# Kernel optimization log

Hardware: AMD Instinct MI355X
Metric: run time of the kernel (lower is better)

## Reference

```python
import jax, jax.numpy as jnp
import numpy as np

EPS = 1e-5  # torch InstanceNorm2d default eps


def instance_norm(x):
    # normalize over spatial dims (H, W) per sample, per channel; affine=False
    mean = jnp.mean(x, axis=(2, 3), keepdims=True)
    var = jnp.var(x, axis=(2, 3), keepdims=True)  # biased var, matching torch
    return (x - mean) * jax.lax.rsqrt(var + EPS)


def conv1x1(x, w, b):
    # x: [B,C,H,W], w: [O,C], b: [O] -> [B,O,H,W]
    return jnp.einsum('oc,bchw->bohw', w, x) + b[None, :, None, None]


def setup_inputs() -> dict:
    key = jax.random.key(0)
    ks = jax.random.split(key, 9)
    B, C, H, W = 4, 64, 96, 96
    fan_out = C  # 1x1 conv: fan_out = out_ch * 1 * 1
    std = float(np.sqrt(2.0 / fan_out))  # kaiming_normal_, mode='fan_out', relu
    x = jax.random.normal(ks[0], (B, C, H, W), dtype=jnp.float32)
    wq = jax.random.normal(ks[1], (C, C), dtype=jnp.float32) * std
    wk = jax.random.normal(ks[2], (C, C), dtype=jnp.float32) * std
    wv = jax.random.normal(ks[3], (C, C), dtype=jnp.float32) * std
    wo = jax.random.normal(ks[4], (C, C), dtype=jnp.float32) * std
    bq = jnp.zeros((C,), dtype=jnp.float32)
    bk = jnp.zeros((C,), dtype=jnp.float32)
    bv = jnp.zeros((C,), dtype=jnp.float32)
    bo = jnp.zeros((C,), dtype=jnp.float32)
    return {"x": x, "wq": wq, "bq": bq, "wk": wk, "bk": bk,
            "wv": wv, "bv": bv, "wo": wo, "bo": bo}


def reference(x, wq, bq, wk, bk, wv, bv, wo, bo):
    B, C, H, W = x.shape
    h = instance_norm(x)
    q = conv1x1(h, wq, bq)  # [B,C,H,W]
    k = conv1x1(h, wk, bk)
    v = conv1x1(h, wv, bv)
    N = H * W
    q = q.reshape(B, C, N).transpose(0, 2, 1)  # [B,N,C]
    k = k.reshape(B, C, N)                     # [B,C,N]
    v = v.reshape(B, C, N).transpose(0, 2, 1)  # [B,N,C]
    scores = jnp.einsum('bnc,bcm->bnm', q, k) * (C ** -0.5)  # [B,N,N]
    attn = jax.nn.softmax(scores, axis=-1)
    o = jnp.einsum('bnm,bmc->bnc', attn, v)  # [B,N,C]
    o = o.reshape(B, H, W, C).transpose(0, 3, 1, 2)  # [B,C,H,W]
    o = conv1x1(o, wo, bo)
    return x + o
```

## Files before the change

### kernel.cpp

```cpp
#include <hip/hip_runtime.h>
#include <stdint.h>

#define BB 4
#define CCH 64
#define NN 9216
#define NTILES 144
#define FTILES 72
#define NCHUNK 3
#define CHUNKK 3072

typedef unsigned short u16;
typedef __attribute__((ext_vector_type(8))) short bhalf8;
typedef __attribute__((ext_vector_type(4))) float f32x4;
typedef __attribute__((ext_vector_type(4))) u16 u16x4;
typedef __attribute__((ext_vector_type(8))) u16 u16x8;
typedef __attribute__((ext_vector_type(2))) unsigned int u32x2;

#define MFMA16(a, b, c) __builtin_amdgcn_mfma_f32_16x16x32_bf16((a), (b), (c), 0, 0, 0)

static __device__ __forceinline__ u16 f2bf(float f) {
  union { float f; unsigned u; } v; v.f = f;
  return (u16)((v.u + 0x7fffu + ((v.u >> 16) & 1u)) >> 16);
}
static __device__ __forceinline__ float bf2f(u16 h) {
  union { unsigned u; float f; } v; v.u = ((unsigned)h) << 16; return v.f;
}
static __device__ __forceinline__ unsigned pk2(float lo, float hi) {
  unsigned a = __float_as_uint(hi) + 0x8000u;
  unsigned b = __float_as_uint(lo) + 0x8000u;
  return __builtin_amdgcn_perm(a, b, 0x07060302u);
}
static __device__ __forceinline__ void glds16(const void* g, void* l) {
  __builtin_amdgcn_global_load_lds(
      (const __attribute__((address_space(1))) unsigned int*)g,
      (__attribute__((address_space(3))) unsigned int*)l, 16, 0, 0);
}

extern "C" __global__ __launch_bounds__(256) void prep_kernel(
    const float* __restrict__ x,
    const float* __restrict__ wq, const float* __restrict__ wk,
    const float* __restrict__ wv, const float* __restrict__ wo,
    float* __restrict__ mean, float* __restrict__ rstd, u16* __restrict__ wbf) {
  if (blockIdx.x >= 256) {
    int i = (blockIdx.x - 256) * 256 + threadIdx.x;
    const float* src = (i < 4096) ? wq : (i < 8192) ? wk : (i < 12288) ? wv : wo;
    wbf[i] = f2bf(src[i & 4095]);
    return;
  }
  int idx = blockIdx.x;
  const float* p = x + (size_t)idx * NN;
  float s = 0.f, ss = 0.f;
  for (int i = threadIdx.x; i < NN; i += 256) { float v = p[i]; s += v; ss += v * v; }
#pragma unroll
  for (int o = 32; o > 0; o >>= 1) { s += __shfl_xor(s, o, 64); ss += __shfl_xor(ss, o, 64); }
  __shared__ float ls[4], lss[4];
  int w = threadIdx.x >> 6;
  if ((threadIdx.x & 63) == 0) { ls[w] = s; lss[w] = ss; }
  __syncthreads();
  if (threadIdx.x == 0) {
    s = ls[0] + ls[1] + ls[2] + ls[3];
    ss = lss[0] + lss[1] + lss[2] + lss[3];
    float m = s * (1.f / NN);
    float var = ss * (1.f / NN) - m * m;
    mean[idx] = m;
    rstd[idx] = rsqrtf(var + 1e-5f);
  }
}

extern "C" __global__ __launch_bounds__(256, 4) void qkv_kernel(
    const float* __restrict__ x,
    const float* __restrict__ mean, const float* __restrict__ rstd,
    const u16* __restrict__ wqb, const u16* __restrict__ wkb, const u16* __restrict__ wvb,
    const float* __restrict__ bq, const float* __restrict__ bk,
    u16* __restrict__ Qt, u16* __restrict__ Kt, u16* __restrict__ Vt) {
  __shared__ u16 hbuf[64 * 72];
  int b = blockIdx.x / NTILES, tile = blockIdx.x % NTILES;
  int n0 = tile * 64;
  int t = threadIdx.x;
  int w = t >> 6, lane = t & 63, q = lane >> 4, ln = lane & 15;
  const float QSCALE = 0.125f * 1.44269504088896340736f;
  const float* mb = mean + b * 64;
  const float* rb_ = rstd + b * 64;
  int nloc = lane;
#pragma unroll
  for (int rep = 0; rep < 4; rep++) {
    int c0 = 16 * w + 4 * rep;
    float h0 = (x[(size_t)(b * 64 + c0 + 0) * NN + n0 + nloc] - mb[c0 + 0]) * rb_[c0 + 0];
    float h1 = (x[(size_t)(b * 64 + c0 + 1) * NN + n0 + nloc] - mb[c0 + 1]) * rb_[c0 + 1];
    float h2 = (x[(size_t)(b * 64 + c0 + 2) * NN + n0 + nloc] - mb[c0 + 2]) * rb_[c0 + 2];
    float h3 = (x[(size_t)(b * 64 + c0 + 3) * NN + n0 + nloc] - mb[c0 + 3]) * rb_[c0 + 3];
    u32x2 hp;
    hp[0] = pk2(h0, h1);
    hp[1] = pk2(h2, h3);
    *(u32x2*)&hbuf[nloc * 72 + c0] = hp;
  }
  __syncthreads();
  int hrow = (16 * w + ln) * 72;
  bhalf8 hb0 = *(const bhalf8*)&hbuf[hrow + q * 8];
  bhalf8 hb1 = *(const bhalf8*)&hbuf[hrow + 32 + q * 8];
  size_t nrow = (size_t)(b * NN + n0 + 16 * w + ln) * 64;
#pragma unroll
  for (int ct = 0; ct < 4; ct++) {
    int wrow = (16 * ct + ln) * 64;
    bhalf8 a0 = *(const bhalf8*)&wqb[wrow + q * 8];
    bhalf8 a1 = *(const bhalf8*)&wqb[wrow + 32 + q * 8];
    f32x4 d = {0.f, 0.f, 0.f, 0.f};
    d = MFMA16(a0, hb0, d);
    d = MFMA16(a1, hb1, d);
    f32x4 b4 = *(const f32x4*)&bq[16 * ct + 4 * q];
    u16x4 pk;
#pragma unroll
    for (int r = 0; r < 4; r++) pk[r] = f2bf((d[r] + b4[r]) * QSCALE);
    *(u16x4*)&Qt[nrow + 16 * ct + 4 * q] = pk;
  }
#pragma unroll
  for (int ct = 0; ct < 4; ct++) {
    int wrow = (16 * ct + ln) * 64;
    bhalf8 a0 = *(const bhalf8*)&wkb[wrow + q * 8];
    bhalf8 a1 = *(const bhalf8*)&wkb[wrow + 32 + q * 8];
    f32x4 d = {0.f, 0.f, 0.f, 0.f};
    d = MFMA16(a0, hb0, d);
    d = MFMA16(a1, hb1, d);
    f32x4 b4 = *(const f32x4*)&bk[16 * ct + 4 * q];
    u16x4 pk;
#pragma unroll
    for (int r = 0; r < 4; r++) pk[r] = f2bf(d[r] + b4[r]);
    *(u16x4*)&Kt[nrow + 16 * ct + 4 * q] = pk;
  }
#pragma unroll
  for (int ct = 0; ct < 4; ct++) {
    int wrow = (16 * ct + ln) * 64;
    bhalf8 b0 = *(const bhalf8*)&wvb[wrow + q * 8];
    bhalf8 b1 = *(const bhalf8*)&wvb[wrow + 32 + q * 8];
    f32x4 d = {0.f, 0.f, 0.f, 0.f};
    d = MFMA16(hb0, b0, d);
    d = MFMA16(hb1, b1, d);
    u16x4 pk;
#pragma unroll
    for (int r = 0; r < 4; r++) pk[r] = f2bf(d[r]);
    *(u16x4*)&Vt[(size_t)(b * 64 + 16 * ct + ln) * NN + n0 + 16 * w + 4 * q] = pk;
  }
}

extern "C" __global__ __launch_bounds__(256, 4) void flash_kernel(
    const u16* __restrict__ Qt, const u16* __restrict__ Kt, const u16* __restrict__ Vt,
    u16* __restrict__ Opart, float* __restrict__ Lsum) {
  __shared__ u16 kbuf[2][64 * 64];
  __shared__ u16 vbuf[2][64 * 64];
  __shared__ u16 pbuf[4][16 * 64];
  int blk = blockIdx.x;
  int b = blk / (FTILES * NCHUNK);
  int rem = blk % (FTILES * NCHUNK);
  int tile = rem / NCHUNK, chunk = rem % NCHUNK;
  int m_start = chunk * CHUNKK;
  int t = threadIdx.x;
  int w = t >> 6, lane = t & 63, q = lane >> 4, ln = lane & 15;
  int n0w = tile * 128 + 32 * w;
  const u16* qp = Qt + (size_t)(b * NN + n0w + ln) * 64 + q * 8;
  bhalf8 qa0 = *(const bhalf8*)qp;
  bhalf8 qa1 = *(const bhalf8*)(qp + 32);
  bhalf8 qb0 = *(const bhalf8*)(qp + 16 * 64);
  bhalf8 qb1 = *(const bhalf8*)(qp + 16 * 64 + 32);
  const short ONE = 0x3F80;
  const bhalf8 ones = {ONE, ONE, ONE, ONE, ONE, ONE, ONE, ONE};
  f32x4 oa[4], ob[4];
  f32x4 lacc_a = {0.f, 0.f, 0.f, 0.f}, lacc_b = {0.f, 0.f, 0.f, 0.f};
#pragma unroll
  for (int i = 0; i < 4; i++) { oa[i] = (f32x4){0.f,0.f,0.f,0.f}; ob[i] = (f32x4){0.f,0.f,0.f,0.f}; }
  u16* pw = pbuf[w];
  int row_s = 16 * w + (lane >> 3);
  int usw = (lane & 7) ^ (row_s & 7);
  const u16* kgp = Kt + ((size_t)b * NN + m_start + row_s) * 64 + usw * 8;
  const u16* vgp = Vt + (size_t)(b * 64 + row_s) * NN + m_start + usw * 8;
  int sbase = (q ^ (ln & 7)) * 8;
  const int NIT = CHUNKK / 64;

  {
    u16* kl = &kbuf[0][w * 1024];
    u16* vl = &vbuf[0][w * 1024];
    glds16(kgp, kl); glds16(kgp + 512, kl + 512);
    glds16(vgp, vl); glds16(vgp + (size_t)8 * NN, vl + 512);
    kgp += 4096; vgp += 64;
  }

#pragma unroll 2
  for (int i = 0; i < NIT; i++) {
    __syncthreads();
    if (i + 1 < NIT) {
      u16* kl = &kbuf[(i + 1) & 1][w * 1024];
      u16* vl = &vbuf[(i + 1) & 1][w * 1024];
      glds16(kgp, kl); glds16(kgp + 512, kl + 512);
      glds16(vgp, vl); glds16(vgp + (size_t)8 * NN, vl + 512);
      kgp += 4096; vgp += 64;
    }
    const u16* kb = kbuf[i & 1];
    const u16* vb = vbuf[i & 1];
#pragma unroll
    for (int p = 0; p < 2; p++) {
      f32x4 s[4];
#pragma unroll
      for (int lm = 0; lm < 2; lm++) {
        int mt = 2 * p + lm;
        int krow = (16 * mt + ln) * 64;
        bhalf8 ka0 = *(const bhalf8*)&kb[krow + sbase];
        bhalf8 ka1 = *(const bhalf8*)&kb[krow + (sbase ^ 32)];
        f32x4 acc = {0.f, 0.f, 0.f, 0.f};
        acc = MFMA16(ka0, qa0, acc);
        acc = MFMA16(ka1, qa1, acc);
        s[2 * lm] = acc;
        f32x4 acc2 = {0.f, 0.f, 0.f, 0.f};
        acc2 = MFMA16(ka0, qb0, acc2);
        acc2 = MFMA16(ka1, qb1, acc2);
        s[2 * lm + 1] = acc2;
      }
#pragma unroll
      for (int lm = 0; lm < 2; lm++) {
        f32x4 pa, pbv;
#pragma unroll
        for (int r = 0; r < 4; r++) {
          pa[r] = __builtin_amdgcn_exp2f(s[2 * lm][r]);
          pbv[r] = __builtin_amdgcn_exp2f(s[2 * lm + 1][r]);
        }
        int ua = (2 * lm + (q >> 1)) ^ (ln & 7);
        int ub = (4 + 2 * lm + (q >> 1)) ^ (ln & 7);
        u32x2 pka, pkb;
        pka[0] = pk2(pa[0], pa[1]);  pka[1] = pk2(pa[2], pa[3]);
        pkb[0] = pk2(pbv[0], pbv[1]); pkb[1] = pk2(pbv[2], pbv[3]);
        *(u32x2*)&pw[ln * 64 + ua * 8 + (q & 1) * 4] = pka;
        *(u32x2*)&pw[ln * 64 + ub * 8 + (q & 1) * 4] = pkb;
      }
      bhalf8 pfa = *(const bhalf8*)&pw[ln * 64 + ((q ^ (ln & 7)) * 8)];
      bhalf8 pfb = *(const bhalf8*)&pw[ln * 64 + (((4 + q) ^ (ln & 7)) * 8)];
      lacc_a = MFMA16(ones, pfa, lacc_a);
      lacc_b = MFMA16(ones, pfb, lacc_b);
#pragma unroll
      for (int ct = 0; ct < 4; ct++) {
        int vrow = (16 * ct + ln) * 64;
        bhalf8 va = *(const bhalf8*)&vb[vrow + (sbase ^ (32 * p))];
        oa[ct] = MFMA16(va, pfa, oa[ct]);
        ob[ct] = MFMA16(va, pfb, ob[ct]);
      }
    }
  }
  size_t pbase = (size_t)blk * (128 * 64);
  int ra = 32 * w + ln, rb = ra + 16;
#pragma unroll
  for (int ct = 0; ct < 4; ct++) {
    u32x2 pka, pkb;
    pka[0] = pk2(oa[ct][0], oa[ct][1]); pka[1] = pk2(oa[ct][2], oa[ct][3]);
    pkb[0] = pk2(ob[ct][0], ob[ct][1]); pkb[1] = pk2(ob[ct][2], ob[ct][3]);
    *(u32x2*)&Opart[pbase + (size_t)ra * 64 + 16 * ct + 4 * q] = pka;
    *(u32x2*)&Opart[pbase + (size_t)rb * 64 + 16 * ct + 4 * q] = pkb;
  }
  if (q == 0) {
    float* lb_ = Lsum + (size_t)blk * 128;
    lb_[ra] = lacc_a[0];
    lb_[rb] = lacc_b[0];
  }
}

extern "C" __global__ __launch_bounds__(256, 4) void out_kernel(
    const float* __restrict__ x, const u16* __restrict__ wob, const float* __restrict__ bo,
    const u16* __restrict__ Opart, const float* __restrict__ Lsum, const float* __restrict__ bv,
    float* __restrict__ out) {
  int b = blockIdx.x / NTILES, tile = blockIdx.x % NTILES;
  int t = threadIdx.x;
  int w = t >> 6, lane = t & 63, q = lane >> 4, ln = lane & 15;
  int n0w = tile * 64 + 16 * w;
  int ptile = tile >> 1;
  int prow = (tile & 1) * 64 + 16 * w + ln;
  int p0 = (b * FTILES + ptile) * NCHUNK;
  float L = 0.f;
  float acc0[8], acc1[8];
#pragma unroll
  for (int j = 0; j < 8; j++) { acc0[j] = 0.f; acc1[j] = 0.f; }
#pragma unroll
  for (int ch = 0; ch < NCHUNK; ch++) {
    L += Lsum[(size_t)(p0 + ch) * 128 + prow];
    const u16* op = Opart + ((size_t)(p0 + ch) * 128 + prow) * 64;
    u16x8 d0 = *(const u16x8*)(op + 8 * q);
    u16x8 d1 = *(const u16x8*)(op + 32 + 8 * q);
#pragma unroll
    for (int j = 0; j < 8; j++) { acc0[j] += bf2f(d0[j]); acc1[j] += bf2f(d1[j]); }
  }
  float rl = 1.0f / L;
  union { u16x8 us; bhalf8 bh; } A0, A1;
#pragma unroll
  for (int j = 0; j < 8; j++) {
    A0.us[j] = f2bf(acc0[j] * rl + bv[8 * q + j]);
    A1.us[j] = f2bf(acc1[j] * rl + bv[32 + 8 * q + j]);
  }
  bhalf8 a0 = A0.bh, a1 = A1.bh;
#pragma unroll
  for (int ct = 0; ct < 4; ct++) {
    int wrow = (16 * ct + ln) * 64;
    bhalf8 b0 = *(const bhalf8*)&wob[wrow + q * 8];
    bhalf8 b1 = *(const bhalf8*)&wob[wrow + 32 + q * 8];
    f32x4 d = {0.f, 0.f, 0.f, 0.f};
    d = MFMA16(a0, b0, d);
    d = MFMA16(a1, b1, d);
    int co = 16 * ct + ln;
    size_t base = (size_t)(b * 64 + co) * NN + n0w + 4 * q;
    f32x4 xv = *(const f32x4*)&x[base];
    float bc = bo[co];
    f32x4 ov;
#pragma unroll
    for (int r = 0; r < 4; r++) ov[r] = xv[r] + bc + d[r];
    *(f32x4*)&out[base] = ov;
  }
}

extern "C" void kernel_launch(void* const* d_in, const int* in_sizes, int n_in,
                              void* d_out, int out_size, void* d_ws, size_t ws_size,
                              hipStream_t stream) {
  (void)in_sizes; (void)n_in; (void)out_size; (void)ws_size;
  const float* x  = (const float*)d_in[0];
  const float* wq = (const float*)d_in[1];
  const float* bq = (const float*)d_in[2];
  const float* wk = (const float*)d_in[3];
  const float* bk = (const float*)d_in[4];
  const float* wv = (const float*)d_in[5];
  const float* bv = (const float*)d_in[6];
  const float* wo = (const float*)d_in[7];
  const float* bo = (const float*)d_in[8];
  float* out = (float*)d_out;
  char* ws = (char*)d_ws;
  float* mean = (float*)ws;
  float* rstd = (float*)(ws + 1024);
  u16* wbf = (u16*)(ws + 2048);
  u16* Qt = (u16*)(ws + 36864);
  u16* Kt = Qt + (size_t)BB * NN * 64;
  u16* Vt = Kt + (size_t)BB * NN * 64;
  u16* Opart = Vt + (size_t)BB * NN * 64;
  float* Lsum = (float*)(Opart + (size_t)BB * FTILES * NCHUNK * 128 * 64);
  const u16* wqb = wbf;
  const u16* wkb = wbf + 4096;
  const u16* wvb = wbf + 8192;
  const u16* wob = wbf + 12288;

  prep_kernel<<<320, 256, 0, stream>>>(x, wq, wk, wv, wo, mean, rstd, wbf);
  qkv_kernel<<<BB * NTILES, 256, 0, stream>>>(x, mean, rstd, wqb, wkb, wvb, bq, bk, Qt, Kt, Vt);
  flash_kernel<<<BB * FTILES * NCHUNK, 256, 0, stream>>>(Qt, Kt, Vt, Opart, Lsum);
  out_kernel<<<BB * NTILES, 256, 0, stream>>>(x, wob, bo, Opart, Lsum, bv, out);
}
```

Before: 220.5 us.

## Enlarge flash query tile to 64 rows per wave with uneven 5-way KV split

Each wave now processes 64 query rows (256 per block) instead of 32, so every K/V tile staged in LDS feeds twice as many MFMAs. This halves the global-to-LDS traffic per unit of compute. The KV range is split into 5 uneven chunks of 28 or 29 iterations to keep the grid large (720 blocks), and the P scratch buffer layout and swizzle are reworked. The cost is far more accumulator registers, which drops launch bounds to 3 waves/SIMD, plus larger partial buffers for the combine kernel.

Measured after the change: 213.1 us. 1.03x faster.

```diff
diff --git a/kernel.cpp b/kernel.cpp
--- a/kernel.cpp
+++ b/kernel.cpp
@@ -5,9 +5,8 @@
 #define CCH 64
 #define NN 9216
 #define NTILES 144
-#define FTILES 72
-#define NCHUNK 3
-#define CHUNKK 3072
+#define FTILES 36
+#define NCHUNK 5
 
 typedef unsigned short u16;
 typedef __attribute__((ext_vector_type(8))) short bhalf8;
@@ -142,38 +141,45 @@
   }
 }
 
-extern "C" __global__ __launch_bounds__(256, 4) void flash_kernel(
+extern "C" __global__ __launch_bounds__(256, 3) void flash_kernel(
     const u16* __restrict__ Qt, const u16* __restrict__ Kt, const u16* __restrict__ Vt,
     u16* __restrict__ Opart, float* __restrict__ Lsum) {
   __shared__ u16 kbuf[2][64 * 64];
   __shared__ u16 vbuf[2][64 * 64];
-  __shared__ u16 pbuf[4][16 * 64];
+  __shared__ u16 pbuf[4][64 * 32];
   int blk = blockIdx.x;
   int b = blk / (FTILES * NCHUNK);
   int rem = blk % (FTILES * NCHUNK);
   int tile = rem / NCHUNK, chunk = rem % NCHUNK;
-  int m_start = chunk * CHUNKK;
+  int it0 = chunk * 28 + (chunk < 4 ? chunk : 4);
+  int nit = 28 + (chunk < 4 ? 1 : 0);
+  int m_start = it0 * 64;
   int t = threadIdx.x;
   int w = t >> 6, lane = t & 63, q = lane >> 4, ln = lane & 15;
-  int n0w = tile * 128 + 32 * w;
-  const u16* qp = Qt + (size_t)(b * NN + n0w + ln) * 64 + q * 8;
-  bhalf8 qa0 = *(const bhalf8*)qp;
-  bhalf8 qa1 = *(const bhalf8*)(qp + 32);
-  bhalf8 qb0 = *(const bhalf8*)(qp + 16 * 64);
-  bhalf8 qb1 = *(const bhalf8*)(qp + 16 * 64 + 32);
+  int n0w = tile * 256 + 64 * w;
+  bhalf8 qf0[4], qf1[4];
+#pragma unroll
+  for (int s = 0; s < 4; s++) {
+    const u16* qp = Qt + (size_t)(b * NN + n0w + 16 * s + ln) * 64 + q * 8;
+    qf0[s] = *(const bhalf8*)qp;
+    qf1[s] = *(const bhalf8*)(qp + 32);
+  }
   const short ONE = 0x3F80;
   const bhalf8 ones = {ONE, ONE, ONE, ONE, ONE, ONE, ONE, ONE};
-  f32x4 oa[4], ob[4];
-  f32x4 lacc_a = {0.f, 0.f, 0.f, 0.f}, lacc_b = {0.f, 0.f, 0.f, 0.f};
-#pragma unroll
-  for (int i = 0; i < 4; i++) { oa[i] = (f32x4){0.f,0.f,0.f,0.f}; ob[i] = (f32x4){0.f,0.f,0.f,0.f}; }
+  f32x4 o[4][4];
+  f32x4 lacc[4];
+#pragma unroll
+  for (int ct = 0; ct < 4; ct++) {
+    lacc[ct] = (f32x4){0.f, 0.f, 0.f, 0.f};
+#pragma unroll
+    for (int s = 0; s < 4; s++) o[ct][s] = (f32x4){0.f, 0.f, 0.f, 0.f};
+  }
   u16* pw = pbuf[w];
   int row_s = 16 * w + (lane >> 3);
   int usw = (lane & 7) ^ (row_s & 7);
   const u16* kgp = Kt + ((size_t)b * NN + m_start + row_s) * 64 + usw * 8;
   const u16* vgp = Vt + (size_t)(b * 64 + row_s) * NN + m_start + usw * 8;
   int sbase = (q ^ (ln & 7)) * 8;
-  const int NIT = CHUNKK / 64;
 
   {
     u16* kl = &kbuf[0][w * 1024];
@@ -183,10 +189,9 @@
     kgp += 4096; vgp += 64;
   }
 
-#pragma unroll 2
-  for (int i = 0; i < NIT; i++) {
+  for (int i = 0; i < nit; i++) {
     __syncthreads();
-    if (i + 1 < NIT) {
+    if (i + 1 < nit) {
       u16* kl = &kbuf[(i + 1) & 1][w * 1024];
       u16* vl = &vbuf[(i + 1) & 1][w * 1024];
       glds16(kgp, kl); glds16(kgp + 512, kl + 512);
@@ -197,65 +202,52 @@
     const u16* vb = vbuf[i & 1];
 #pragma unroll
     for (int p = 0; p < 2; p++) {
-      f32x4 s[4];
 #pragma unroll
       for (int lm = 0; lm < 2; lm++) {
-        int mt = 2 * p + lm;
-        int krow = (16 * mt + ln) * 64;
+        int krow = (16 * (2 * p + lm) + ln) * 64;
         bhalf8 ka0 = *(const bhalf8*)&kb[krow + sbase];
         bhalf8 ka1 = *(const bhalf8*)&kb[krow + (sbase ^ 32)];
-        f32x4 acc = {0.f, 0.f, 0.f, 0.f};
-        acc = MFMA16(ka0, qa0, acc);
-        acc = MFMA16(ka1, qa1, acc);
-        s[2 * lm] = acc;
-        f32x4 acc2 = {0.f, 0.f, 0.f, 0.f};
-        acc2 = MFMA16(ka0, qb0, acc2);
-        acc2 = MFMA16(ka1, qb1, acc2);
-        s[2 * lm + 1] = acc2;
+        int uw = (((2 * lm + (q >> 1)) ^ ((ln >> 1) & 3)) << 3) + ((q & 1) << 2);
+#pragma unroll
+        for (int s = 0; s < 4; s++) {
+          f32x4 acc = {0.f, 0.f, 0.f, 0.f};
+          acc = MFMA16(ka0, qf0[s], acc);
+          acc = MFMA16(ka1, qf1[s], acc);
+          f32x4 pv;
+#pragma unroll
+          for (int r = 0; r < 4; r++) pv[r] = __builtin_amdgcn_exp2f(acc[r]);
+          u32x2 pk;
+          pk[0] = pk2(pv[0], pv[1]);
+          pk[1] = pk2(pv[2], pv[3]);
+          *(u32x2*)&pw[(16 * s + ln) * 32 + uw] = pk;
+        }
       }
-#pragma unroll
-      for (int lm = 0; lm < 2; lm++) {
-        f32x4 pa, pbv;
-#pragma unroll
-        for (int r = 0; r < 4; r++) {
-          pa[r] = __builtin_amdgcn_exp2f(s[2 * lm][r]);
-          pbv[r] = __builtin_amdgcn_exp2f(s[2 * lm + 1][r]);
-        }
-        int ua = (2 * lm + (q >> 1)) ^ (ln & 7);
-        int ub = (4 + 2 * lm + (q >> 1)) ^ (ln & 7);
-        u32x2 pka, pkb;
-        pka[0] = pk2(pa[0], pa[1]);  pka[1] = pk2(pa[2], pa[3]);
-        pkb[0] = pk2(pbv[0], pbv[1]); pkb[1] = pk2(pbv[2], pbv[3]);
-        *(u32x2*)&pw[ln * 64 + ua * 8 + (q & 1) * 4] = pka;
-        *(u32x2*)&pw[ln * 64 + ub * 8 + (q & 1) * 4] = pkb;
-      }
-      bhalf8 pfa = *(const bhalf8*)&pw[ln * 64 + ((q ^ (ln & 7)) * 8)];
-      bhalf8 pfb = *(const bhalf8*)&pw[ln * 64 + (((4 + q) ^ (ln & 7)) * 8)];
-      lacc_a = MFMA16(ones, pfa, lacc_a);
-      lacc_b = MFMA16(ones, pfb, lacc_b);
+      int ur = ((q ^ ((ln >> 1) & 3)) << 3);
+      bhalf8 pf[4];
+#pragma unroll
+      for (int s = 0; s < 4; s++) pf[s] = *(const bhalf8*)&pw[(16 * s + ln) * 32 + ur];
+#pragma unroll
+      for (int s = 0; s < 4; s++) lacc[s] = MFMA16(ones, pf[s], lacc[s]);
 #pragma unroll
       for (int ct = 0; ct < 4; ct++) {
-        int vrow = (16 * ct + ln) * 64;
-        bhalf8 va = *(const bhalf8*)&vb[vrow + (sbase ^ (32 * p))];
-        oa[ct] = MFMA16(va, pfa, oa[ct]);
-        ob[ct] = MFMA16(va, pfb, ob[ct]);
+        bhalf8 va = *(const bhalf8*)&vb[(16 * ct + ln) * 64 + (sbase ^ (32 * p))];
+#pragma unroll
+        for (int s = 0; s < 4; s++) o[ct][s] = MFMA16(va, pf[s], o[ct][s]);
       }
     }
   }
-  size_t pbase = (size_t)blk * (128 * 64);
-  int ra = 32 * w + ln, rb = ra + 16;
-#pragma unroll
-  for (int ct = 0; ct < 4; ct++) {
-    u32x2 pka, pkb;
-    pka[0] = pk2(oa[ct][0], oa[ct][1]); pka[1] = pk2(oa[ct][2], oa[ct][3]);
-    pkb[0] = pk2(ob[ct][0], ob[ct][1]); pkb[1] = pk2(ob[ct][2], ob[ct][3]);
-    *(u32x2*)&Opart[pbase + (size_t)ra * 64 + 16 * ct + 4 * q] = pka;
-    *(u32x2*)&Opart[pbase + (size_t)rb * 64 + 16 * ct + 4 * q] = pkb;
-  }
-  if (q == 0) {
-    float* lb_ = Lsum + (size_t)blk * 128;
-    lb_[ra] = lacc_a[0];
-    lb_[rb] = lacc_b[0];
+  size_t pbase = (size_t)blk * (256 * 64);
+#pragma unroll
+  for (int s = 0; s < 4; s++) {
+    int row = 64 * w + 16 * s + ln;
+#pragma unroll
+    for (int ct = 0; ct < 4; ct++) {
+      u32x2 pk;
+      pk[0] = pk2(o[ct][s][0], o[ct][s][1]);
+      pk[1] = pk2(o[ct][s][2], o[ct][s][3]);
+      *(u32x2*)&Opart[pbase + (size_t)row * 64 + 16 * ct + 4 * q] = pk;
+    }
+    if (q == 0) Lsum[(size_t)blk * 256 + row] = lacc[s][0];
   }
 }
 
@@ -267,8 +259,8 @@
   int t = threadIdx.x;
   int w = t >> 6, lane = t & 63, q = lane >> 4, ln = lane & 15;
   int n0w = tile * 64 + 16 * w;
-  int ptile = tile >> 1;
-  int prow = (tile & 1) * 64 + 16 * w + ln;
+  int ptile = tile >> 2;
+  int prow = (tile & 3) * 64 + 16 * w + ln;
   int p0 = (b * FTILES + ptile) * NCHUNK;
   float L = 0.f;
   float acc0[8], acc1[8];
@@ -276,8 +268,8 @@
   for (int j = 0; j < 8; j++) { acc0[j] = 0.f; acc1[j] = 0.f; }
 #pragma unroll
   for (int ch = 0; ch < NCHUNK; ch++) {
-    L += Lsum[(size_t)(p0 + ch) * 128 + prow];
-    const u16* op = Opart + ((size_t)(p0 + ch) * 128 + prow) * 64;
+    L += Lsum[(size_t)(p0 + ch) * 256 + prow];
+    const u16* op = Opart + ((size_t)(p0 + ch) * 256 + prow) * 64;
     u16x8 d0 = *(const u16x8*)(op + 8 * q);
     u16x8 d1 = *(const u16x8*)(op + 32 + 8 * q);
 #pragma unroll
@@ -332,7 +324,7 @@
   u16* Kt = Qt + (size_t)BB * NN * 64;
   u16* Vt = Kt + (size_t)BB * NN * 64;
   u16* Opart = Vt + (size_t)BB * NN * 64;
-  float* Lsum = (float*)(Opart + (size_t)BB * FTILES * NCHUNK * 128 * 64);
+  float* Lsum = (float*)(Opart + (size_t)BB * FTILES * NCHUNK * 256 * 64);
   const u16* wqb = wbf;
   const u16* wkb = wbf + 4096;
   const u16* wvb = wbf + 8192;
```
